# Performance work log

Measured on AMD Instinct MI355X. Metric: run time of the kernel, lower is better.

The kernel has to match this reference:

```python
import jax, jax.numpy as jnp
import numpy as np


def _lstm_scan(x_bte, W_ih, W_hh, b_ih, b_hh, h0, c0):
    """Single-layer LSTM over time (torch gate order i,f,g,o).
    x_bte: [B,T,E]; returns (h_seq [B,T,H], (h_T, c_T))."""
    H = h0.shape[-1]
    # precompute input projections for all timesteps: [T,B,4H]
    xp = jnp.einsum('bte,ge->tbg', x_bte, W_ih) + (b_ih + b_hh)

    def step(carry, xg):
        h, c = carry
        gates = xg + h @ W_hh.T  # [B,4H]
        i, f, g, o = jnp.split(gates, 4, axis=-1)
        c = jax.nn.sigmoid(f) * c + jax.nn.sigmoid(i) * jnp.tanh(g)
        h = jax.nn.sigmoid(o) * jnp.tanh(c)
        return (h, c), h

    (hT, cT), h_seq = jax.lax.scan(step, (h0, c0), xp)
    return jnp.transpose(h_seq, (1, 0, 2)), (hT, cT)


def setup_inputs() -> dict:
    key = jax.random.key(0)
    ks = jax.random.split(key, 10)
    V, E, H = 32000, 256, 512
    B, S, T = 64, 64, 32
    s = 0.02
    return {
        'src': jax.random.randint(ks[0], (B, S), 0, V),
        'tgt': jax.random.randint(ks[1], (B, T), 0, V),
        'enc_emb': jax.random.normal(ks[2], (V, E), jnp.float32) * s,
        'dec_emb': jax.random.normal(ks[3], (V, E), jnp.float32) * s,
        'enc_Wih': jax.random.normal(ks[4], (4 * H, E), jnp.float32) * s,
        'enc_Whh': jax.random.normal(ks[5], (4 * H, H), jnp.float32) * s,
        'enc_bih': jnp.zeros((4 * H,), jnp.float32),
        'enc_bhh': jnp.zeros((4 * H,), jnp.float32),
        'dec_Wih': jax.random.normal(ks[6], (4 * H, E), jnp.float32) * s,
        'dec_Whh': jax.random.normal(ks[7], (4 * H, H), jnp.float32) * s,
        'dec_bih': jnp.zeros((4 * H,), jnp.float32),
        'dec_bhh': jnp.zeros((4 * H,), jnp.float32),
        'fc_W': jax.random.normal(ks[8], (V, H), jnp.float32) * s,
        'fc_b': jnp.zeros((V,), jnp.float32),
    }


def reference(src, tgt, enc_emb, dec_emb, enc_Wih, enc_Whh, enc_bih, enc_bhh,
              dec_Wih, dec_Whh, dec_bih, dec_bhh, fc_W, fc_b):
    B, T = tgt.shape
    H = enc_Whh.shape[-1]
    V = fc_W.shape[0]
    h0 = jnp.zeros((B, H), jnp.float32)
    c0 = jnp.zeros((B, H), jnp.float32)

    # Encoder (dropout=0.0 -> identity)
    emb_src = enc_emb[src]  # [B,S,E]
    _, (hT, cT) = _lstm_scan(emb_src, enc_Wih, enc_Whh, enc_bih, enc_bhh, h0, c0)
    hT = jax.lax.stop_gradient(hT)  # .detach() in torch source
    cT = jax.lax.stop_gradient(cT)

    # Decoder, teacher_forcing_ratio=1.0 -> inputs are tgt[:, :-1]
    emb_tgt = dec_emb[tgt[:, :-1]]  # [B,T-1,E]
    h_seq, _ = _lstm_scan(emb_tgt, dec_Wih, dec_Whh, dec_bih, dec_bhh, hT, cT)
    logits = jnp.einsum('bth,vh->btv', h_seq, fc_W) + fc_b  # [B,T-1,V]

    # outputs[:,0] stays zeros as in torch code
    outputs = jnp.concatenate([jnp.zeros((B, 1, V), jnp.float32), logits], axis=1)
    return outputs
```

## Files before the change

### kernel.cpp

```cpp
#include <hip/hip_runtime.h>
#include <cstdint>
#include <cstddef>

#define NB    64
#define SENC  64
#define TDEC  31
#define EDIM  256
#define HDIM  512
#define VOCAB 32000
#define MROWS (NB * TDEC)
#define MPAD  2048
#define NBLK  256
#define KW    32

#define OFF_HTA  0
#define OFF_HTB  (OFF_HTA + HDIM * NB * 4)
#define OFF_XPE  (OFF_HTB + HDIM * NB * 4)
#define OFF_XPD  (OFF_XPE + 256 * SENC * 8 * NB * 4)
#define OFF_HS   (OFF_XPD + 256 * TDEC * 8 * NB * 4)
#define OFF_FCW  (OFF_HS + MPAD * HDIM * 2)

typedef __attribute__((ext_vector_type(8))) short bf16x8;
typedef __attribute__((ext_vector_type(4))) float f32x4;

__device__ __forceinline__ float sigf(float x) { return 1.0f / (1.0f + __expf(-x)); }
__device__ __forceinline__ float tanhfast(float x) {
  return 1.0f - 2.0f / (__expf(2.0f * x) + 1.0f);
}
__device__ __forceinline__ unsigned short f2bf(float x) {
  unsigned int u = __float_as_uint(x);
  u += 0x7fffu + ((u >> 16) & 1u);
  return (unsigned short)(u >> 16);
}
__device__ __forceinline__ unsigned pack2(float a, float b) {
  return (unsigned)f2bf(a) | ((unsigned)f2bf(b) << 16);
}

__global__ __launch_bounds__(256) void setup_k(const float* __restrict__ fc_W,
                                               unsigned short* __restrict__ fcw,
                                               float* __restrict__ hTA,
                                               unsigned short* __restrict__ hs,
                                               float* __restrict__ out) {
  const int gt = blockIdx.x * 256 + threadIdx.x;
  const int GSZ = 2048 * 256;
  const float4* s4 = (const float4*)fc_W;
  uint4* d4 = (uint4*)fcw;
  for (int i = gt; i < (VOCAB * HDIM / 8); i += GSZ) {
    float4 x = s4[2 * i], y = s4[2 * i + 1];
    uint4 v;
    v.x = pack2(x.x, x.y); v.y = pack2(x.z, x.w);
    v.z = pack2(y.x, y.y); v.w = pack2(y.z, y.w);
    d4[i] = v;
  }
  float4 z4 = make_float4(0.f, 0.f, 0.f, 0.f);
  for (int j = gt; j < NB * (VOCAB / 4); j += GSZ) {
    int b = j / (VOCAB / 4), q = j - b * (VOCAB / 4);
    ((float4*)out)[(size_t)b * (32 * (VOCAB / 4)) + q] = z4;
  }
  if (gt < HDIM * NB / 4) ((float4*)hTA)[gt] = z4;
  if (gt < (MPAD - MROWS) * HDIM / 8) {
    uint4 uz = {0u, 0u, 0u, 0u};
    ((uint4*)(hs + (size_t)MROWS * HDIM))[gt] = uz;
  }
}

__device__ void xp_phase(const int* idxmat, int istride, int S,
                         const float* emb, const float* Wih,
                         const float* bih, const float* bhh,
                         float* xp_out, int bid, int tid,
                         float* W_lds, float* pbuf, float* bias_lds) {
  const int lane = tid & 63;
  const int w = tid >> 6;
  {
    int r = tid >> 5;
    int e0 = (tid & 31) * 8;
    int row_g = (r >> 1) * HDIM + bid * 2 + (r & 1);
    const float* sp = Wih + (size_t)row_g * EDIM + e0;
    *(float4*)&W_lds[r * EDIM + e0]     = *(const float4*)sp;
    *(float4*)&W_lds[r * EDIM + e0 + 4] = *(const float4*)(sp + 4);
    if (tid < 8) {
      int rg = (tid >> 1) * HDIM + bid * 2 + (tid & 1);
      bias_lds[tid] = bih[rg] + bhh[rg];
    }
  }
  __syncthreads();
  for (int s = 0; s < S; ++s) {
    int idx = idxmat[lane * istride + s];
    const float* xrow = emb + (size_t)idx * EDIM;
    float acc[8];
#pragma unroll
    for (int r = 0; r < 8; ++r) acc[r] = 0.0f;
    for (int e = w * 64; e < w * 64 + 64; e += 4) {
      float4 xv = *(const float4*)&xrow[e];
#pragma unroll
      for (int r = 0; r < 8; ++r) {
        float4 wv = *(const float4*)&W_lds[r * EDIM + e];
        acc[r] += wv.x * xv.x + wv.y * xv.y + wv.z * xv.z + wv.w * xv.w;
      }
    }
#pragma unroll
    for (int r = 0; r < 8; ++r) pbuf[(w * 8 + r) * 64 + lane] = acc[r];
    __syncthreads();
    if (tid < 128) {
      int unit = tid >> 6, b = tid & 63;
#pragma unroll
      for (int gate = 0; gate < 4; ++gate) {
        int r = gate * 2 + unit;
        float v = bias_lds[r];
#pragma unroll
        for (int ww = 0; ww < 4; ++ww) v += pbuf[(ww * 8 + r) * 64 + b];
        xp_out[((size_t)(bid * S + s) * 8 + r) * 64 + b] = v;
      }
    }
    __syncthreads();
  }
}

struct XpParams {
  const int* src; const int* tgt;
  const float* enc_emb; const float* dec_emb;
  const float* enc_Wih; const float* enc_bih; const float* enc_bhh;
  const float* dec_Wih; const float* dec_bih; const float* dec_bhh;
  float* xpe; float* xpd;
};

__global__ __launch_bounds__(256) void xp_k(XpParams p) {
  __shared__ __align__(16) float W_lds[8 * EDIM];
  __shared__ float pbuf[32 * 64];
  __shared__ float bias_lds[8];
  const int bid = blockIdx.x;
  if (bid < 256)
    xp_phase(p.src, SENC, SENC, p.enc_emb, p.enc_Wih, p.enc_bih, p.enc_bhh,
             p.xpe, bid, threadIdx.x, W_lds, pbuf, bias_lds);
  else
    xp_phase(p.tgt, 32, TDEC, p.dec_emb, p.dec_Wih, p.dec_bih, p.dec_bhh,
             p.xpd, bid - 256, threadIdx.x, W_lds, pbuf, bias_lds);
}

__device__ __forceinline__ void grid_barrier(unsigned* flags, unsigned gen) {
  asm volatile("s_waitcnt vmcnt(0)" ::: "memory");
  __syncthreads();
  const int tid = threadIdx.x;
  if (tid == 0)
    __hip_atomic_store(&flags[blockIdx.x], gen, __ATOMIC_RELAXED,
                       __HIP_MEMORY_SCOPE_AGENT);
  if (tid < 64) {
    const unsigned* f4 = flags + tid * 4;
    for (;;) {
      unsigned a = __hip_atomic_load(&f4[0], __ATOMIC_RELAXED, __HIP_MEMORY_SCOPE_AGENT);
      unsigned b = __hip_atomic_load(&f4[1], __ATOMIC_RELAXED, __HIP_MEMORY_SCOPE_AGENT);
      unsigned c = __hip_atomic_load(&f4[2], __ATOMIC_RELAXED, __HIP_MEMORY_SCOPE_AGENT);
      unsigned d = __hip_atomic_load(&f4[3], __ATOMIC_RELAXED, __HIP_MEMORY_SCOPE_AGENT);
      unsigned m0 = a < b ? a : b;
      unsigned m1 = c < d ? c : d;
      unsigned m = m0 < m1 ? m0 : m1;
      if (__all((int)(m >= gen))) break;
      __builtin_amdgcn_s_sleep(1);
    }
  }
  __syncthreads();
}

__device__ __forceinline__ void recur_phase(const float* Whh, const float* xp,
                            int S, int gen0, int last_phase, int bid, int tid,
                            float* pbuf, float* c_lds,
                            float*& hp, float*& hn,
                            unsigned short* hs_or_null, unsigned* flags) {
  const int lane = tid & 63;
  const int wu = __builtin_amdgcn_readfirstlane(tid >> 6);
  const int j0 = bid * 2;

  const float* Wr[8];
#pragma unroll
  for (int r = 0; r < 8; ++r)
    Wr[r] = Whh + (size_t)((r >> 1) * HDIM + j0 + (r & 1)) * HDIM + wu * KW;

  const int unit = tid >> 6;
  const int b = tid & 63;
  float xg[4];
  if (tid < 128) {
#pragma unroll
    for (int gate = 0; gate < 4; ++gate) {
      int r = gate * 2 + unit;
      xg[gate] = xp[((size_t)(bid * S) * 8 + r) * 64 + b];
    }
  }

  for (int s = 0; s < S; ++s) {
    float hreg[KW];
    const float* hb = hp + (size_t)wu * KW * 64 + lane;
#pragma unroll
    for (int k = 0; k < KW; ++k)
      hreg[k] = __hip_atomic_load(&hb[k * 64], __ATOMIC_RELAXED,
                                  __HIP_MEMORY_SCOPE_AGENT);

    float acc[8];
#pragma unroll
    for (int r = 0; r < 8; ++r) acc[r] = 0.0f;
#pragma unroll
    for (int k = 0; k < KW; ++k) {
#pragma unroll
      for (int r = 0; r < 8; ++r) acc[r] += Wr[r][k] * hreg[k];
    }
#pragma unroll
    for (int r = 0; r < 8; ++r) pbuf[(wu * 8 + r) * 64 + lane] = acc[r];
    __syncthreads();

    float xgn[4];
    if (tid < 128) {
      float g[4];
#pragma unroll
      for (int gate = 0; gate < 4; ++gate) {
        int r = gate * 2 + unit;
        float v = xg[gate];
#pragma unroll
        for (int ww = 0; ww < 16; ++ww) v += pbuf[(ww * 8 + r) * 64 + b];
        g[gate] = v;
      }
      float c = c_lds[unit * 64 + b];
      float iv = sigf(g[0]), fv = sigf(g[1]);
      float gv = tanhfast(g[2]), ov = sigf(g[3]);
      c = fv * c + iv * gv;
      float h = ov * tanhfast(c);
      c_lds[unit * 64 + b] = c;
      __hip_atomic_store(&hn[(j0 + unit) * 64 + b], h, __ATOMIC_RELAXED,
                         __HIP_MEMORY_SCOPE_AGENT);
      if (hs_or_null)
        hs_or_null[((size_t)b * TDEC + s) * HDIM + j0 + unit] = f2bf(h);
      int sn = (s + 1 < S) ? s + 1 : s;
#pragma unroll
      for (int gate = 0; gate < 4; ++gate) {
        int r = gate * 2 + unit;
        xgn[gate] = xp[((size_t)(bid * S + sn) * 8 + r) * 64 + b];
      }
    }
    if (!(last_phase && s == S - 1))
      grid_barrier(flags, (unsigned)(gen0 + s + 1));
    if (tid < 128) {
#pragma unroll
      for (int gate = 0; gate < 4; ++gate) xg[gate] = xgn[gate];
    }
    float* tmp = hp; hp = hn; hn = tmp;
  }
}

struct RecurParams {
  const float* enc_Whh; const float* dec_Whh;
  const float* xpe; const float* xpd;
  float* hTA; float* hTB;
  unsigned short* hs;
  unsigned* flags;
};

__global__ __launch_bounds__(1024, 1) void recur_coop(RecurParams p) {
  __shared__ float pbuf[128 * 64];
  __shared__ float c_lds[2 * 64];
  const int tid = threadIdx.x;
  const int bid = blockIdx.x;
  if (tid < 128) c_lds[tid] = 0.0f;
  __syncthreads();
  float* hp = p.hTA;
  float* hn = p.hTB;
  recur_phase(p.enc_Whh, p.xpe, SENC, 0, 0, bid, tid, pbuf, c_lds,
              hp, hn, nullptr, p.flags);
  recur_phase(p.dec_Whh, p.xpd, TDEC, SENC, 1, bid, tid, pbuf, c_lds,
              hp, hn, p.hs, p.flags);
}

__global__ __launch_bounds__(256) void fc_gemm(const unsigned short* __restrict__ A,
                                               const unsigned short* __restrict__ Bm,
                                               const float* __restrict__ bias,
                                               float* __restrict__ out) {
  __shared__ __align__(16) unsigned short As[128 * 32];
  __shared__ __align__(16) unsigned short Bs[128 * 32];
  const int tid = threadIdx.x;
  const int lane = tid & 63;
  const int w = tid >> 6;
  const int m0 = blockIdx.y * 128;
  const int n0 = blockIdx.x * 128;
  const int wm = (w >> 1) * 64;
  const int wn = (w & 1) * 64;
  const int ml = lane & 15;
  const int kq = (lane >> 4) * 8;

  f32x4 acc[4][4] = {};

  for (int k0 = 0; k0 < HDIM; k0 += 32) {
    for (int c = tid; c < 512; c += 256) {
      int row = c >> 2;
      int ko = (c & 3) * 8;
      *(uint4*)&As[c * 8] = *(const uint4*)(A + (size_t)(m0 + row) * HDIM + k0 + ko);
      *(uint4*)&Bs[c * 8] = *(const uint4*)(Bm + (size_t)(n0 + row) * HDIM + k0 + ko);
    }
    __syncthreads();
    bf16x8 fa[4], fb[4];
#pragma unroll
    for (int i = 0; i < 4; ++i)
      fa[i] = *(const bf16x8*)&As[(wm + 16 * i + ml) * 32 + kq];
#pragma unroll
    for (int j = 0; j < 4; ++j)
      fb[j] = *(const bf16x8*)&Bs[(wn + 16 * j + ml) * 32 + kq];
#pragma unroll
    for (int i = 0; i < 4; ++i)
#pragma unroll
      for (int j = 0; j < 4; ++j)
        acc[i][j] = __builtin_amdgcn_mfma_f32_16x16x32_bf16(fa[i], fb[j], acc[i][j], 0, 0, 0);
    __syncthreads();
  }

  const int rq = (lane >> 4) * 4;
#pragma unroll
  for (int j = 0; j < 4; ++j) {
    int n = n0 + wn + 16 * j + ml;
    float bv = bias[n];
#pragma unroll
    for (int i = 0; i < 4; ++i) {
#pragma unroll
      for (int r = 0; r < 4; ++r) {
        int m = m0 + wm + 16 * i + rq + r;
        if (m < MROWS) {
          int b = m / TDEC;
          int t = m - b * TDEC;
          out[((size_t)(b * 32 + t + 1)) * VOCAB + n] = acc[i][j][r] + bv;
        }
      }
    }
  }
}

extern "C" void kernel_launch(void* const* d_in, const int* in_sizes, int n_in,
                              void* d_out, int out_size, void* d_ws, size_t ws_size,
                              hipStream_t stream) {
  (void)in_sizes; (void)n_in; (void)out_size; (void)ws_size;
  const int* src      = (const int*)d_in[0];
  const int* tgt      = (const int*)d_in[1];
  const float* enc_emb = (const float*)d_in[2];
  const float* dec_emb = (const float*)d_in[3];
  const float* enc_Wih = (const float*)d_in[4];
  const float* enc_Whh = (const float*)d_in[5];
  const float* enc_bih = (const float*)d_in[6];
  const float* enc_bhh = (const float*)d_in[7];
  const float* dec_Wih = (const float*)d_in[8];
  const float* dec_Whh = (const float*)d_in[9];
  const float* dec_bih = (const float*)d_in[10];
  const float* dec_bhh = (const float*)d_in[11];
  const float* fc_W    = (const float*)d_in[12];
  const float* fc_b    = (const float*)d_in[13];
  char* ws = (char*)d_ws;
  float* hTA = (float*)(ws + OFF_HTA);
  float* hTB = (float*)(ws + OFF_HTB);
  float* xpe = (float*)(ws + OFF_XPE);
  float* xpd = (float*)(ws + OFF_XPD);
  unsigned short* hs  = (unsigned short*)(ws + OFF_HS);
  unsigned short* fcw = (unsigned short*)(ws + OFF_FCW);
  unsigned* flags = (unsigned*)(ws + OFF_HS + (size_t)MROWS * HDIM * 2);
  float* out = (float*)d_out;

  hipLaunchKernelGGL(setup_k, dim3(2048), dim3(256), 0, stream, fc_W, fcw, hTA, hs, out);

  XpParams xq = { src, tgt, enc_emb, dec_emb, enc_Wih, enc_bih, enc_bhh,
                  dec_Wih, dec_bih, dec_bhh, xpe, xpd };
  hipLaunchKernelGGL(xp_k, dim3(512), dim3(256), 0, stream, xq);

  RecurParams rp = { enc_Whh, dec_Whh, xpe, xpd, hTA, hTB, hs, flags };
  void* args[] = { &rp };
  hipLaunchCooperativeKernel((const void*)recur_coop, dim3(NBLK), dim3(1024), args, 0, stream);

  hipLaunchKernelGGL(fc_gemm, dim3(VOCAB / 128, MPAD / 128), dim3(256), 0, stream,
                     hs, fcw, fc_b, out);
}
```

Measured before the change: 2.434 ms.

## Use per-timestep hidden-state slots and split gate reduction across more threads

Replaces the ping-pong h buffers with one slot per timestep (96 slots), so each step reads a fresh address. Plain loads then stay correct without device-scope atomic loads, since stale cache lines cannot alias. The 16-way partial-sum reduction of the gates is spread over 512 threads into a shared gsum array instead of 128 threads each doing 64 adds. This costs an extra __syncthreads per step and more workspace memory, and it relies on the cache-coherence assumptions holding for non-atomic loads.

```diff
diff --git a/kernel.cpp b/kernel.cpp
--- a/kernel.cpp
+++ b/kernel.cpp
@@ -13,9 +13,11 @@
 #define NBLK  256
 #define KW    32
 
-#define OFF_HTA  0
-#define OFF_HTB  (OFF_HTA + HDIM * NB * 4)
-#define OFF_XPE  (OFF_HTB + HDIM * NB * 4)
+#define HSLOT (HDIM * NB)
+#define NSLOT 96
+
+#define OFF_HH   0
+#define OFF_XPE  (OFF_HH + NSLOT * HSLOT * 4)
 #define OFF_XPD  (OFF_XPE + 256 * SENC * 8 * NB * 4)
 #define OFF_HS   (OFF_XPD + 256 * TDEC * 8 * NB * 4)
 #define OFF_FCW  (OFF_HS + MPAD * HDIM * 2)
@@ -38,7 +40,7 @@
 
 __global__ __launch_bounds__(256) void setup_k(const float* __restrict__ fc_W,
                                                unsigned short* __restrict__ fcw,
-                                               float* __restrict__ hTA,
+                                               float* __restrict__ hh,
                                                unsigned short* __restrict__ hs,
                                                float* __restrict__ out) {
   const int gt = blockIdx.x * 256 + threadIdx.x;
@@ -57,7 +59,7 @@
     int b = j / (VOCAB / 4), q = j - b * (VOCAB / 4);
     ((float4*)out)[(size_t)b * (32 * (VOCAB / 4)) + q] = z4;
   }
-  if (gt < HDIM * NB / 4) ((float4*)hTA)[gt] = z4;
+  if (gt < HSLOT / 4) ((float4*)hh)[gt] = z4;
   if (gt < (MPAD - MROWS) * HDIM / 8) {
     uint4 uz = {0u, 0u, 0u, 0u};
     ((uint4*)(hs + (size_t)MROWS * HDIM))[gt] = uz;
@@ -163,8 +165,8 @@
 
 __device__ __forceinline__ void recur_phase(const float* Whh, const float* xp,
                             int S, int gen0, int last_phase, int bid, int tid,
-                            float* pbuf, float* c_lds,
-                            float*& hp, float*& hn,
+                            float* pbuf, float* gsum, float* c_lds,
+                            float* hh,
                             unsigned short* hs_or_null, unsigned* flags) {
   const int lane = tid & 63;
   const int wu = __builtin_amdgcn_readfirstlane(tid >> 6);
@@ -187,12 +189,13 @@
   }
 
   for (int s = 0; s < S; ++s) {
+    const float* hp = hh + (size_t)(gen0 + s) * HSLOT;
+    float* hn = hh + (size_t)(gen0 + s + 1) * HSLOT;
+
     float hreg[KW];
     const float* hb = hp + (size_t)wu * KW * 64 + lane;
 #pragma unroll
-    for (int k = 0; k < KW; ++k)
-      hreg[k] = __hip_atomic_load(&hb[k * 64], __ATOMIC_RELAXED,
-                                  __HIP_MEMORY_SCOPE_AGENT);
+    for (int k = 0; k < KW; ++k) hreg[k] = hb[k * 64];
 
     float acc[8];
 #pragma unroll
@@ -204,19 +207,23 @@
     }
 #pragma unroll
     for (int r = 0; r < 8; ++r) pbuf[(wu * 8 + r) * 64 + lane] = acc[r];
+    __syncthreads();
+
+    if (tid < 512) {
+      int row = tid >> 6, bb = tid & 63;
+      float v = 0.0f;
+#pragma unroll
+      for (int ww = 0; ww < 16; ++ww) v += pbuf[(ww * 8 + row) * 64 + bb];
+      gsum[row * 64 + bb] = v;
+    }
     __syncthreads();
 
     float xgn[4];
     if (tid < 128) {
       float g[4];
 #pragma unroll
-      for (int gate = 0; gate < 4; ++gate) {
-        int r = gate * 2 + unit;
-        float v = xg[gate];
-#pragma unroll
-        for (int ww = 0; ww < 16; ++ww) v += pbuf[(ww * 8 + r) * 64 + b];
-        g[gate] = v;
-      }
+      for (int gate = 0; gate < 4; ++gate)
+        g[gate] = xg[gate] + gsum[(gate * 2 + unit) * 64 + b];
       float c = c_lds[unit * 64 + b];
       float iv = sigf(g[0]), fv = sigf(g[1]);
       float gv = tanhfast(g[2]), ov = sigf(g[3]);
@@ -240,31 +247,29 @@
 #pragma unroll
       for (int gate = 0; gate < 4; ++gate) xg[gate] = xgn[gate];
     }
-    float* tmp = hp; hp = hn; hn = tmp;
   }
 }
 
 struct RecurParams {
   const float* enc_Whh; const float* dec_Whh;
   const float* xpe; const float* xpd;
-  float* hTA; float* hTB;
+  float* hh;
   unsigned short* hs;
   unsigned* flags;
 };
 
 __global__ __launch_bounds__(1024, 1) void recur_coop(RecurParams p) {
   __shared__ float pbuf[128 * 64];
+  __shared__ float gsum[8 * 64];
   __shared__ float c_lds[2 * 64];
   const int tid = threadIdx.x;
   const int bid = blockIdx.x;
   if (tid < 128) c_lds[tid] = 0.0f;
   __syncthreads();
-  float* hp = p.hTA;
-  float* hn = p.hTB;
-  recur_phase(p.enc_Whh, p.xpe, SENC, 0, 0, bid, tid, pbuf, c_lds,
-              hp, hn, nullptr, p.flags);
-  recur_phase(p.dec_Whh, p.xpd, TDEC, SENC, 1, bid, tid, pbuf, c_lds,
-              hp, hn, p.hs, p.flags);
+  recur_phase(p.enc_Whh, p.xpe, SENC, 0, 0, bid, tid, pbuf, gsum, c_lds,
+              p.hh, nullptr, p.flags);
+  recur_phase(p.dec_Whh, p.xpd, TDEC, SENC, 1, bid, tid, pbuf, gsum, c_lds,
+              p.hh, p.hs, p.flags);
 }
 
 __global__ __launch_bounds__(256) void fc_gemm(const unsigned short* __restrict__ A,
@@ -347,8 +352,7 @@
   const float* fc_W    = (const float*)d_in[12];
   const float* fc_b    = (const float*)d_in[13];
   char* ws = (char*)d_ws;
-  float* hTA = (float*)(ws + OFF_HTA);
-  float* hTB = (float*)(ws + OFF_HTB);
+  float* hh  = (float*)(ws + OFF_HH);
   float* xpe = (float*)(ws + OFF_XPE);
   float* xpd = (float*)(ws + OFF_XPD);
   unsigned short* hs  = (unsigned short*)(ws + OFF_HS);
@@ -356,13 +360,13 @@
   unsigned* flags = (unsigned*)(ws + OFF_HS + (size_t)MROWS * HDIM * 2);
   float* out = (float*)d_out;
 
-  hipLaunchKernelGGL(setup_k, dim3(2048), dim3(256), 0, stream, fc_W, fcw, hTA, hs, out);
+  hipLaunchKernelGGL(setup_k, dim3(2048), dim3(256), 0, stream, fc_W, fcw, hh, hs, out);
 
   XpParams xq = { src, tgt, enc_emb, dec_emb, enc_Wih, enc_bih, enc_bhh,
                   dec_Wih, dec_bih, dec_bhh, xpe, xpd };
   hipLaunchKernelGGL(xp_k, dim3(512), dim3(256), 0, stream, xq);
 
-  RecurParams rp = { enc_Whh, dec_Whh, xpe, xpd, hTA, hTB, hs, flags };
+  RecurParams rp = { enc_Whh, dec_Whh, xpe, xpd, hh, hs, flags };
   void* args[] = { &rp };
   hipLaunchCooperativeKernel((const void*)recur_coop, dim3(NBLK), dim3(1024), args, 0, stream);
 
```

After: 2.407 ms. Within noise of the previous version (-1.1%).
